# Optimization experiments

Measured on AMD Instinct MI355X. Metric: run time of the kernel, lower is better.

## Reference

```python
import jax, jax.numpy as jnp
import numpy as np

N_ = 512   # batch / num users
M_ = 254   # num UAV nodes -> size S = M_ + 2 = 256
D_ = 2     # coordinate dim
H_ = 128   # pointer-net hidden dim


def setup_inputs() -> dict:
    key = jax.random.key(0)
    ks = jax.random.split(key, 7)
    s = 0.1
    return {
        "outputs": jax.random.normal(ks[0], (2 * N_ + M_, D_), dtype=jnp.float32),
        "W_embed": jax.random.normal(ks[1], (D_, H_), dtype=jnp.float32) * s,
        "b_embed": jnp.zeros((H_,), jnp.float32),
        "lstm_Wi": jax.random.normal(ks[2], (H_, 4 * H_), dtype=jnp.float32) * s,
        "lstm_Wh": jax.random.normal(ks[3], (H_, 4 * H_), dtype=jnp.float32) * s,
        "lstm_b": jnp.zeros((4 * H_,), jnp.float32),
        "att_W1": jax.random.normal(ks[4], (H_, H_), dtype=jnp.float32) * s,
        "att_W2": jax.random.normal(ks[5], (H_, H_), dtype=jnp.float32) * s,
        "att_v": jax.random.normal(ks[6], (H_,), dtype=jnp.float32) * s,
        "N": N_,
    }


def _rgnn_loss(outputs, W_embed, b_embed, lstm_Wi, lstm_Wh, lstm_b,
               att_W1, att_W2, att_v, N):
    D = outputs.shape[1]
    H = W_embed.shape[1]
    M = outputs.shape[0] - 2 * N
    users_src = outputs[:N][:, None, :]                         # (B,1,D)
    users_dst = outputs[N:2 * N][:, None, :]                    # (B,1,D)
    uav_nodes = jnp.broadcast_to(outputs[2 * N:][None, :, :], (N, M, D))
    uav_graph = jnp.concatenate([users_src, uav_nodes, users_dst], axis=1)  # (B,S,D)
    B, S = uav_graph.shape[0], uav_graph.shape[1]
    NEG = jnp.float32(-np.inf)

    # pointer-net: node embeddings and step-independent attention projection
    e_all = uav_graph @ W_embed + b_embed                       # (B,S,H)
    W1e = jnp.einsum('bsh,hk->bsk', e_all, att_W1)              # (B,S,H)
    rows = jnp.arange(B)

    mask0 = jnp.zeros((B, S), jnp.float32).at[:, 0].set(NEG)
    x0 = uav_graph[:, 0, :]                                     # start at src
    carry0 = (x0, x0,
              jnp.zeros((B, H), jnp.float32), jnp.zeros((B, H), jnp.float32),
              mask0, jnp.zeros((B,), jnp.float32))

    def step(carry, k):
        x, Y0, h, c, mask, max_dist = carry
        # dst node blocked only at step 0, re-opened afterwards
        mask = mask.at[:, -1].set(jnp.where(k == 0, NEG, 0.0))
        # LSTM cell on embedded current node
        e_x = x @ W_embed + b_embed                             # (B,H)
        gates = e_x @ lstm_Wi + h @ lstm_Wh + lstm_b            # (B,4H)
        i, f, g, o = jnp.split(gates, 4, axis=1)
        c = jax.nn.sigmoid(f) * c + jax.nn.sigmoid(i) * jnp.tanh(g)
        h = jax.nn.sigmoid(o) * jnp.tanh(c)
        # additive attention pointer logits
        q = h @ att_W2                                          # (B,H)
        logits = jnp.tanh(W1e + q[:, None, :]) @ att_v + mask   # (B,S)
        logits = jax.lax.stop_gradient(logits)                  # output.detach()
        idx = jnp.argmax(logits, axis=1)                        # (B,)
        Y1 = uav_graph[rows, idx]                               # (B,D)
        dist = jnp.sqrt(jnp.sum((Y1 - Y0) ** 2, axis=1) + 1e-12)
        max_dist = jnp.maximum(max_dist, dist)
        mask = mask.at[rows, idx].add(NEG)
        mask = jnp.where((idx == S)[:, None], NEG, mask)
        return (Y1, Y1, h, c, mask, max_dist), None

    (_, _, _, _, _, max_dist), _ = jax.lax.scan(step, carry0, jnp.arange(S))
    return max_dist.mean()


def reference(outputs, W_embed, b_embed, lstm_Wi, lstm_Wh, lstm_b,
              att_W1, att_W2, att_v, N):
    return _rgnn_loss(outputs, W_embed, b_embed, lstm_Wi, lstm_Wh, lstm_b,
                      att_W1, att_W2, att_v, N)
```

## Files before the change

kernel.cpp:

```cpp
#include <hip/hip_runtime.h>
#include <math.h>

#define NB   512
#define MM   254
#define SS   256
#define HH   128
#define RTOT 1278
#define NBLK 256

#define C2   2.885390081777927f
#define C1   1.442695040888963f

__device__ __forceinline__ float rcpf(float x)  { return __builtin_amdgcn_rcpf(x); }
__device__ __forceinline__ float exp2f_(float x){ return __builtin_amdgcn_exp2f(x); }
__device__ __forceinline__ float sigm2(float x) { return rcpf(1.0f + exp2f_(-C1 * x)); }
__device__ __forceinline__ float tanh2(float x) { return 1.0f - 2.0f * rcpf(1.0f + exp2f_(C2 * x)); }

__device__ __forceinline__ float dot8(float4 aA, float4 aB, float4 bA, float4 bB,
                                      float4 vA, float4 vB, float4 qA, float4 qB,
                                      float pxn, float pyn) {
  float acc = 0.f;
  acc = fmaf(vA.x, rcpf(1.0f + exp2f_(fmaf(pxn, aA.x, fmaf(pyn, bA.x, qA.x)))), acc);
  acc = fmaf(vA.y, rcpf(1.0f + exp2f_(fmaf(pxn, aA.y, fmaf(pyn, bA.y, qA.y)))), acc);
  acc = fmaf(vA.z, rcpf(1.0f + exp2f_(fmaf(pxn, aA.z, fmaf(pyn, bA.z, qA.z)))), acc);
  acc = fmaf(vA.w, rcpf(1.0f + exp2f_(fmaf(pxn, aA.w, fmaf(pyn, bA.w, qA.w)))), acc);
  acc = fmaf(vB.x, rcpf(1.0f + exp2f_(fmaf(pxn, aB.x, fmaf(pyn, bB.x, qB.x)))), acc);
  acc = fmaf(vB.y, rcpf(1.0f + exp2f_(fmaf(pxn, aB.y, fmaf(pyn, bB.y, qB.y)))), acc);
  acc = fmaf(vB.z, rcpf(1.0f + exp2f_(fmaf(pxn, aB.z, fmaf(pyn, bB.z, qB.z)))), acc);
  acc = fmaf(vB.w, rcpf(1.0f + exp2f_(fmaf(pxn, aB.w, fmaf(pyn, bB.w, qB.w)))), acc);
  return acc;
}

__global__ __launch_bounds__(512) void coef_k(
    const float* __restrict__ Wemb, const float* __restrict__ bemb,
    const float* __restrict__ Wi, const float* __restrict__ W1,
    const float* __restrict__ lb, float* __restrict__ coef)
{
  int j = threadIdx.x;
  float a = 0.f, b = 0.f, c = 0.f;
#pragma unroll 8
  for (int h = 0; h < HH; ++h) {
    float w = Wi[(size_t)h * 512 + j];
    a = fmaf(Wemb[h], w, a);
    b = fmaf(Wemb[HH + h], w, b);
    c = fmaf(bemb[h], w, c);
  }
  coef[j] = a; coef[512 + j] = b; coef[1024 + j] = c + lb[j];
  if (j < HH) {
    float a1 = 0.f, b1 = 0.f, c1 = 0.f;
#pragma unroll 8
    for (int h = 0; h < HH; ++h) {
      float w = W1[(size_t)h * HH + j];
      a1 = fmaf(Wemb[h], w, a1);
      b1 = fmaf(Wemb[HH + h], w, b1);
      c1 = fmaf(bemb[h], w, c1);
    }
    coef[1536 + j] = C2 * a1; coef[1664 + j] = C2 * b1; coef[1792 + j] = C2 * c1;
  }
}

__global__ __launch_bounds__(128) void transpose_k(
    const float* __restrict__ Wh, const float* __restrict__ W2,
    float* __restrict__ WhT, float* __restrict__ W2T)
{
  int bidx = blockIdx.x;
  int k = threadIdx.x;
  if (bidx < 512) WhT[(size_t)bidx * 128 + k] = Wh[(size_t)k * 512 + bidx];
  else {
    int j = bidx - 512;
    W2T[(size_t)j * 128 + k] = W2[(size_t)k * 128 + j];
  }
}

__global__ __attribute__((amdgpu_waves_per_eu(4, 4)))
__launch_bounds__(1024) void decode_k(
    const float* __restrict__ outputs, const float* __restrict__ WhT,
    const float* __restrict__ Wh, const float* __restrict__ W2T,
    const float* __restrict__ av, const float* __restrict__ coef,
    float* __restrict__ maxd_out)
{
  const int t = threadIdx.x;
  const int bid = blockIdx.x;

  __shared__ float WhL[64][512];
  __shared__ float posU[2 * MM];
  __shared__ float dstS[2][2];
  __shared__ float curP[2][2];
  __shared__ __align__(16) float hS[2][HH];
  __shared__ __align__(16) float qC[2][HH];
  __shared__ float C1sS[HH];
  __shared__ __align__(16) float A1sS[HH], B1sS[HH], vS2[HH];
  __shared__ __align__(16) float AiS[512], BiS[512], CiS[512];
  __shared__ float pS[2][2][512];
  __shared__ float lgS[2][SS];
  __shared__ int   actS[2][254];
  __shared__ int   cntS[2];

  const int gh  = (t >> 5) & 1;
  const int gj  = ((t >> 6) << 5) | (t & 31);
  const int cg  = t >> 9;
  const int cj  = (t >> 2) & 127;
  const int ckq = t & 3;

  const int eg  = t >> 9;
  const int tg  = t & 511;
  const int ewv = tg >> 6;
  const int eul = (tg >> 4) & 3;
  const int esl = tg & 15;

  for (int i = t; i < 64 * 512; i += 1024) ((float*)WhL)[i] = Wh[64 * 512 + i];
  for (int i = t; i < 2 * MM; i += 1024)   posU[i] = outputs[4 * NB + i];
  if (t < HH) {
    C1sS[t] = coef[1792 + t];
    A1sS[t] = coef[1536 + t];
    B1sS[t] = coef[1664 + t];
    vS2[t]  = -2.0f * av[t];
  }
  if (t < 512) { AiS[t] = coef[t]; BiS[t] = coef[512 + t]; CiS[t] = coef[1024 + t]; }
  if (t < 256) { int gg = t >> 7, j = t & 127; hS[gg][j] = 0.f; }
  if (t < 254) actS[0][t] = t + 1;
  else if (t >= 512 && t < 766) actS[1][t - 512] = t - 511;
  if (t == 0) {
    cntS[0] = 254;
    dstS[0][0] = outputs[2 * (NB + bid)]; dstS[0][1] = outputs[2 * (NB + bid) + 1];
    curP[0][0] = outputs[2 * bid];        curP[0][1] = outputs[2 * bid + 1];
  }
  if (t == 512) {
    cntS[1] = 254;
    dstS[1][0] = outputs[2 * (NB + bid + NBLK)];
    dstS[1][1] = outputs[2 * (NB + bid + NBLK) + 1];
    curP[1][0] = outputs[2 * (bid + NBLK)];
    curP[1][1] = outputs[2 * (bid + NBLK) + 1];
  }
  __syncthreads();

  float px = 0.f, py = 0.f, md = 0.f;
  if (t == 0)   { px = curP[0][0]; py = curP[0][1]; }
  if (t == 512) { px = curP[1][0]; py = curP[1][1]; }

  float creg = 0.f;

  for (int k = 0; k < SS; ++k) {
    {
      const float4* wg4 = (const float4*)(WhT + (size_t)gj * 128 + gh * 32);
      const float*  wl  = &WhL[gh * 32][gj];
      const float4* hb0g = (const float4*)(&hS[0][gh * 32]);
      const float4* hb1g = (const float4*)(&hS[1][gh * 32]);
      const float4* hb0l = (const float4*)(&hS[0][64 + gh * 32]);
      const float4* hb1l = (const float4*)(&hS[1][64 + gh * 32]);
      float a0G = 0.f, a1G = 0.f, a0L = 0.f, a1L = 0.f;
      float4 wb[4];
#pragma unroll
      for (int i = 0; i < 4; ++i) wb[i] = wg4[i];
#pragma unroll
      for (int i = 0; i < 4; ++i) {
        float4 h0 = hb0l[i], h1 = hb1l[i];
        float wa = wl[(size_t)(4 * i) * 512];
        float wbv = wl[(size_t)(4 * i + 1) * 512];
        float wc = wl[(size_t)(4 * i + 2) * 512];
        float wd = wl[(size_t)(4 * i + 3) * 512];
        a0L = fmaf(h0.x, wa, a0L); a0L = fmaf(h0.y, wbv, a0L);
        a0L = fmaf(h0.z, wc, a0L); a0L = fmaf(h0.w, wd, a0L);
        a1L = fmaf(h1.x, wa, a1L); a1L = fmaf(h1.y, wbv, a1L);
        a1L = fmaf(h1.z, wc, a1L); a1L = fmaf(h1.w, wd, a1L);
      }
#pragma unroll
      for (int i = 0; i < 4; ++i) {
        float4 h0 = hb0g[i], h1 = hb1g[i], w = wb[i];
        a0G = fmaf(h0.x, w.x, a0G); a0G = fmaf(h0.y, w.y, a0G);
        a0G = fmaf(h0.z, w.z, a0G); a0G = fmaf(h0.w, w.w, a0G);
        a1G = fmaf(h1.x, w.x, a1G); a1G = fmaf(h1.y, w.y, a1G);
        a1G = fmaf(h1.z, w.z, a1G); a1G = fmaf(h1.w, w.w, a1G);
      }
#pragma unroll
      for (int i = 0; i < 4; ++i) wb[i] = wg4[4 + i];
#pragma unroll
      for (int i = 4; i < 8; ++i) {
        float4 h0 = hb0l[i], h1 = hb1l[i];
        float wa = wl[(size_t)(4 * i) * 512];
        float wbv = wl[(size_t)(4 * i + 1) * 512];
        float wc = wl[(size_t)(4 * i + 2) * 512];
        float wd = wl[(size_t)(4 * i + 3) * 512];
        a0L = fmaf(h0.x, wa, a0L); a0L = fmaf(h0.y, wbv, a0L);
        a0L = fmaf(h0.z, wc, a0L); a0L = fmaf(h0.w, wd, a0L);
        a1L = fmaf(h1.x, wa, a1L); a1L = fmaf(h1.y, wbv, a1L);
        a1L = fmaf(h1.z, wc, a1L); a1L = fmaf(h1.w, wd, a1L);
      }
#pragma unroll
      for (int i = 0; i < 4; ++i) {
        float4 h0 = hb0g[4 + i], h1 = hb1g[4 + i], w = wb[i];
        a0G = fmaf(h0.x, w.x, a0G); a0G = fmaf(h0.y, w.y, a0G);
        a0G = fmaf(h0.z, w.z, a0G); a0G = fmaf(h0.w, w.w, a0G);
        a1G = fmaf(h1.x, w.x, a1G); a1G = fmaf(h1.y, w.y, a1G);
        a1G = fmaf(h1.z, w.z, a1G); a1G = fmaf(h1.w, w.w, a1G);
      }
      pS[0][gh][gj] = a0G + a0L;
      pS[1][gh][gj] = a1G + a1L;
    }
    __syncthreads();

    if (t < 256) {
      int g = t >> 7, jj = t & 127;
      float pxc = curP[g][0], pyc = curP[g][1];
      float ei = fmaf(pxc, AiS[jj],       fmaf(pyc, BiS[jj],       CiS[jj]))       + (pS[g][0][jj]       + pS[g][1][jj]);
      float ef = fmaf(pxc, AiS[128 + jj], fmaf(pyc, BiS[128 + jj], CiS[128 + jj])) + (pS[g][0][128 + jj] + pS[g][1][128 + jj]);
      float eg2 = fmaf(pxc, AiS[256 + jj], fmaf(pyc, BiS[256 + jj], CiS[256 + jj])) + (pS[g][0][256 + jj] + pS[g][1][256 + jj]);
      float eo = fmaf(pxc, AiS[384 + jj], fmaf(pyc, BiS[384 + jj], CiS[384 + jj])) + (pS[g][0][384 + jj] + pS[g][1][384 + jj]);
      float iv = sigm2(ei), fv = sigm2(ef), gv = tanh2(eg2), ov = sigm2(eo);
      float cn = fv * creg + iv * gv;
      creg = cn;
      hS[g][jj] = ov * tanh2(cn);
    }
    __syncthreads();

    {
      const float4* w4 = (const float4*)(W2T + (size_t)cj * 128 + ckq * 32);
      const float4* h4 = (const float4*)(&hS[cg][ckq * 32]);
      float p0 = 0.f, p1 = 0.f;
#pragma unroll
      for (int i = 0; i < 8; ++i) {
        float4 w = w4[i], h = h4[i];
        p0 = fmaf(h.x, w.x, p0); p1 = fmaf(h.y, w.y, p1);
        p0 = fmaf(h.z, w.z, p0); p1 = fmaf(h.w, w.w, p1);
      }
      float p = p0 + p1;
      p += __shfl_xor(p, 1);
      p += __shfl_xor(p, 2);
      if (ckq == 0) qC[cg][cj] = fmaf(C2, p, C1sS[cj]);
    }
    __syncthreads();

    {
      int cnt = cntS[eg];
      int cntEff = cnt + (k > 0 ? 1 : 0);
      const float4* a4 = (const float4*)(&A1sS[esl * 8]);
      const float4* b4 = (const float4*)(&B1sS[esl * 8]);
      const float4* v4 = (const float4*)(&vS2[esl * 8]);
      const float4* q4 = (const float4*)(&qC[eg][esl * 8]);
      float4 aA = a4[0], aB = a4[1];
      float4 bA = b4[0], bB = b4[1];
      float4 vA = v4[0], vB = v4[1];
      float4 qA = q4[0], qB = q4[1];
#pragma unroll 2
      for (int c = 0; c < 8; ++c) {
        int u = ewv * 4 + eul + 32 * c;
        if (u < cntEff) {
          int s = (u == cnt) ? 255 : actS[eg][u];
          float pxn, pyn;
          if (s == 255) { pxn = dstS[eg][0]; pyn = dstS[eg][1]; }
          else          { pxn = posU[2 * (s - 1)]; pyn = posU[2 * (s - 1) + 1]; }
          float acc = dot8(aA, aB, bA, bB, vA, vB, qA, qB, pxn, pyn);
          acc += __shfl_xor(acc, 1);
          acc += __shfl_xor(acc, 2);
          acc += __shfl_xor(acc, 4);
          acc += __shfl_xor(acc, 8);
          if (esl == 0) lgS[eg][u] = acc;
        }
      }
    }
    __syncthreads();

    if ((t < 64) || (t >= 512 && t < 576)) {
      int g = t >> 9;
      int lane = t & 63;
      int cnt = cntS[g];
      int cntEff = cnt + (k > 0 ? 1 : 0);
      float val = -INFINITY;
      unsigned key = 0xFFFFFFFFu;
#pragma unroll 2
      for (int c = 0; c < 4; ++c) {
        int u = lane + 64 * c;
        if (u < cntEff) {
          float v2 = lgS[g][u];
          int s = (u == cnt) ? 255 : actS[g][u];
          unsigned k2 = ((unsigned)s << 16) | (unsigned)u;
          if (v2 > val || (v2 == val && k2 < key)) { val = v2; key = k2; }
        }
      }
#pragma unroll
      for (int off = 1; off < 64; off <<= 1) {
        float v2 = __shfl_xor(val, off);
        unsigned k2 = __shfl_xor(key, off);
        if (v2 > val || (v2 == val && k2 < key)) { val = v2; key = k2; }
      }
      if (lane == 0) {
        int s   = (int)(key >> 16);
        int pos = (int)(key & 0xFFFFu);
        float nx, ny;
        if (s == 255) { nx = dstS[g][0]; ny = dstS[g][1]; }
        else          { nx = posU[2 * (s - 1)]; ny = posU[2 * (s - 1) + 1]; }
        float dx = nx - px, dy = ny - py;
        float d = sqrtf(dx * dx + dy * dy + 1e-12f);
        if (d > md) md = d;
        px = nx; py = ny;
        curP[g][0] = nx; curP[g][1] = ny;
        if (s != 255) { actS[g][pos] = actS[g][cnt - 1]; cntS[g] = cnt - 1; }
      }
    }
    __syncthreads();
  }

  if (t == 0)   maxd_out[bid] = md;
  if (t == 512) maxd_out[bid + NBLK] = md;
}

__global__ __launch_bounds__(512) void reduce_k(const float* __restrict__ maxd,
                                               float* __restrict__ out)
{
  __shared__ float s[512];
  int t = threadIdx.x;
  s[t] = maxd[t];
  __syncthreads();
  for (int off = 256; off > 0; off >>= 1) {
    if (t < off) s[t] += s[t + off];
    __syncthreads();
  }
  if (t == 0) out[0] = s[0] * (1.0f / 512.0f);
}

extern "C" void kernel_launch(void* const* d_in, const int* in_sizes, int n_in,
                              void* d_out, int out_size, void* d_ws, size_t ws_size,
                              hipStream_t stream) {
  const float* outputs = (const float*)d_in[0];
  const float* Wemb    = (const float*)d_in[1];
  const float* bemb    = (const float*)d_in[2];
  const float* Wi      = (const float*)d_in[3];
  const float* Wh      = (const float*)d_in[4];
  const float* lb      = (const float*)d_in[5];
  const float* W1      = (const float*)d_in[6];
  const float* W2      = (const float*)d_in[7];
  const float* av      = (const float*)d_in[8];

  float* ws   = (float*)d_ws;
  float* coef = ws;
  float* WhT  = coef + 2048;
  float* W2T  = WhT + (size_t)512 * 128;
  float* maxd = W2T + (size_t)128 * 128;

  hipLaunchKernelGGL(coef_k, dim3(1), dim3(512), 0, stream,
                     Wemb, bemb, Wi, W1, lb, coef);
  hipLaunchKernelGGL(transpose_k, dim3(640), dim3(128), 0, stream, Wh, W2, WhT, W2T);
  hipLaunchKernelGGL(decode_k, dim3(NBLK), dim3(1024), 0, stream,
                     outputs, WhT, Wh, W2T, av, coef, maxd);
  hipLaunchKernelGGL(reduce_k, dim3(1), dim3(512), 0, stream, maxd, (float*)d_out);
}
```

Measured before the change: 2.600 ms.

## Repartition attention logits: per-thread candidates over hidden quarters, drop shuffle reductions

The attention-logit stage changes from 16 lanes per candidate with a four-level shuffle reduction to each thread handling two candidates over a 32-wide slice of the hidden dimension. Partial sums go to a shared 4xS buffer and are summed in the argmax stage. This removes the cross-lane shuffles and the idle lanes caused by the masked candidate count. In exchange it adds shared-memory traffic and a different summation order, which can flip argmax ties on near-equal logits.

```diff
diff --git a/kernel.cpp b/kernel.cpp
--- a/kernel.cpp
+++ b/kernel.cpp
@@ -15,21 +15,6 @@
 __device__ __forceinline__ float exp2f_(float x){ return __builtin_amdgcn_exp2f(x); }
 __device__ __forceinline__ float sigm2(float x) { return rcpf(1.0f + exp2f_(-C1 * x)); }
 __device__ __forceinline__ float tanh2(float x) { return 1.0f - 2.0f * rcpf(1.0f + exp2f_(C2 * x)); }
-
-__device__ __forceinline__ float dot8(float4 aA, float4 aB, float4 bA, float4 bB,
-                                      float4 vA, float4 vB, float4 qA, float4 qB,
-                                      float pxn, float pyn) {
-  float acc = 0.f;
-  acc = fmaf(vA.x, rcpf(1.0f + exp2f_(fmaf(pxn, aA.x, fmaf(pyn, bA.x, qA.x)))), acc);
-  acc = fmaf(vA.y, rcpf(1.0f + exp2f_(fmaf(pxn, aA.y, fmaf(pyn, bA.y, qA.y)))), acc);
-  acc = fmaf(vA.z, rcpf(1.0f + exp2f_(fmaf(pxn, aA.z, fmaf(pyn, bA.z, qA.z)))), acc);
-  acc = fmaf(vA.w, rcpf(1.0f + exp2f_(fmaf(pxn, aA.w, fmaf(pyn, bA.w, qA.w)))), acc);
-  acc = fmaf(vB.x, rcpf(1.0f + exp2f_(fmaf(pxn, aB.x, fmaf(pyn, bB.x, qB.x)))), acc);
-  acc = fmaf(vB.y, rcpf(1.0f + exp2f_(fmaf(pxn, aB.y, fmaf(pyn, bB.y, qB.y)))), acc);
-  acc = fmaf(vB.z, rcpf(1.0f + exp2f_(fmaf(pxn, aB.z, fmaf(pyn, bB.z, qB.z)))), acc);
-  acc = fmaf(vB.w, rcpf(1.0f + exp2f_(fmaf(pxn, aB.w, fmaf(pyn, bB.w, qB.w)))), acc);
-  return acc;
-}
 
 __global__ __launch_bounds__(512) void coef_k(
     const float* __restrict__ Wemb, const float* __restrict__ bemb,
@@ -92,7 +77,7 @@
   __shared__ __align__(16) float A1sS[HH], B1sS[HH], vS2[HH];
   __shared__ __align__(16) float AiS[512], BiS[512], CiS[512];
   __shared__ float pS[2][2][512];
-  __shared__ float lgS[2][SS];
+  __shared__ float lp[2][4][SS];
   __shared__ int   actS[2][254];
   __shared__ int   cntS[2];
 
@@ -101,12 +86,9 @@
   const int cg  = t >> 9;
   const int cj  = (t >> 2) & 127;
   const int ckq = t & 3;
-
-  const int eg  = t >> 9;
-  const int tg  = t & 511;
-  const int ewv = tg >> 6;
-  const int eul = (tg >> 4) & 3;
-  const int esl = tg & 15;
+  const int lg  = t >> 9;
+  const int lhq = (t >> 7) & 3;
+  const int lu  = t & 127;
 
   for (int i = t; i < 64 * 512; i += 1024) ((float*)WhL)[i] = Wh[64 * 512 + i];
   for (int i = t; i < 2 * MM; i += 1024)   posU[i] = outputs[4 * NB + i];
@@ -231,32 +213,44 @@
     __syncthreads();
 
     {
-      int cnt = cntS[eg];
+      int cnt = cntS[lg];
       int cntEff = cnt + (k > 0 ? 1 : 0);
-      const float4* a4 = (const float4*)(&A1sS[esl * 8]);
-      const float4* b4 = (const float4*)(&B1sS[esl * 8]);
-      const float4* v4 = (const float4*)(&vS2[esl * 8]);
-      const float4* q4 = (const float4*)(&qC[eg][esl * 8]);
-      float4 aA = a4[0], aB = a4[1];
-      float4 bA = b4[0], bB = b4[1];
-      float4 vA = v4[0], vB = v4[1];
-      float4 qA = q4[0], qB = q4[1];
-#pragma unroll 2
-      for (int c = 0; c < 8; ++c) {
-        int u = ewv * 4 + eul + 32 * c;
-        if (u < cntEff) {
-          int s = (u == cnt) ? 255 : actS[eg][u];
-          float pxn, pyn;
-          if (s == 255) { pxn = dstS[eg][0]; pyn = dstS[eg][1]; }
-          else          { pxn = posU[2 * (s - 1)]; pyn = posU[2 * (s - 1) + 1]; }
-          float acc = dot8(aA, aB, bA, bB, vA, vB, qA, qB, pxn, pyn);
-          acc += __shfl_xor(acc, 1);
-          acc += __shfl_xor(acc, 2);
-          acc += __shfl_xor(acc, 4);
-          acc += __shfl_xor(acc, 8);
-          if (esl == 0) lgS[eg][u] = acc;
+      int u0 = lu, u1 = lu + 128;
+      bool e0 = u0 < cntEff, e1 = u1 < cntEff;
+      float px0 = 0.f, py0 = 0.f, px1 = 0.f, py1 = 0.f;
+      if (e0) {
+        int s0 = (u0 == cnt) ? 255 : actS[lg][u0];
+        if (s0 == 255) { px0 = dstS[lg][0]; py0 = dstS[lg][1]; }
+        else           { px0 = posU[2 * (s0 - 1)]; py0 = posU[2 * (s0 - 1) + 1]; }
+      }
+      if (e1) {
+        int s1 = (u1 == cnt) ? 255 : actS[lg][u1];
+        if (s1 == 255) { px1 = dstS[lg][0]; py1 = dstS[lg][1]; }
+        else           { px1 = posU[2 * (s1 - 1)]; py1 = posU[2 * (s1 - 1) + 1]; }
+      }
+      const float4* a14 = (const float4*)(&A1sS[lhq * 32]);
+      const float4* b14 = (const float4*)(&B1sS[lhq * 32]);
+      const float4* qc4 = (const float4*)(&qC[lg][lhq * 32]);
+      const float4* vv4 = (const float4*)(&vS2[lhq * 32]);
+      float c00 = 0.f, c01 = 0.f, c10 = 0.f, c11 = 0.f;
+#pragma unroll 4
+      for (int i = 0; i < 8; ++i) {
+        float4 a = a14[i], b = b14[i], qc = qc4[i], v = vv4[i];
+        if (e0) {
+          c00 = fmaf(v.x, rcpf(1.0f + exp2f_(fmaf(px0, a.x, fmaf(py0, b.x, qc.x)))), c00);
+          c01 = fmaf(v.y, rcpf(1.0f + exp2f_(fmaf(px0, a.y, fmaf(py0, b.y, qc.y)))), c01);
+          c00 = fmaf(v.z, rcpf(1.0f + exp2f_(fmaf(px0, a.z, fmaf(py0, b.z, qc.z)))), c00);
+          c01 = fmaf(v.w, rcpf(1.0f + exp2f_(fmaf(px0, a.w, fmaf(py0, b.w, qc.w)))), c01);
         }
-      }
+        if (e1) {
+          c10 = fmaf(v.x, rcpf(1.0f + exp2f_(fmaf(px1, a.x, fmaf(py1, b.x, qc.x)))), c10);
+          c11 = fmaf(v.y, rcpf(1.0f + exp2f_(fmaf(px1, a.y, fmaf(py1, b.y, qc.y)))), c11);
+          c10 = fmaf(v.z, rcpf(1.0f + exp2f_(fmaf(px1, a.z, fmaf(py1, b.z, qc.z)))), c10);
+          c11 = fmaf(v.w, rcpf(1.0f + exp2f_(fmaf(px1, a.w, fmaf(py1, b.w, qc.w)))), c11);
+        }
+      }
+      if (e0) lp[lg][lhq][u0] = c00 + c01;
+      if (e1) lp[lg][lhq][u1] = c10 + c11;
     }
     __syncthreads();
 
@@ -271,7 +265,7 @@
       for (int c = 0; c < 4; ++c) {
         int u = lane + 64 * c;
         if (u < cntEff) {
-          float v2 = lgS[g][u];
+          float v2 = (lp[g][0][u] + lp[g][1][u]) + (lp[g][2][u] + lp[g][3][u]);
           int s = (u == cnt) ? 255 : actS[g][u];
           unsigned k2 = ((unsigned)s << 16) | (unsigned)u;
           if (v2 > val || (v2 == val && k2 < key)) { val = v2; key = k2; }
```

New measurement: 2.122 ms. -18.4%, faster.
